# Kernel tuning notes

Hardware: AMD Instinct MI355X
Metric: run time of the kernel (lower is better)

The kernel has to match this reference:

```python
import math
import jax, jax.numpy as jnp
import numpy as np

B, L, D, H, NL, V = 4, 1024, 1024, 16, 8, 32000
HD = D // H
EPS = 1e-5


def _sinusoidal_pe(length, dim):
    pos = jnp.arange(length, dtype=jnp.float32)[:, None]
    div = jnp.exp(jnp.arange(0, dim, 2, dtype=jnp.float32) * (-math.log(10000.0) / dim))
    pe = jnp.zeros((length, dim), dtype=jnp.float32)
    pe = pe.at[:, 0::2].set(jnp.sin(pos * div))
    pe = pe.at[:, 1::2].set(jnp.cos(pos * div))
    return pe


def _layer_norm(x, scale, bias):
    mu = jnp.mean(x, axis=-1, keepdims=True)
    var = jnp.mean(jnp.square(x - mu), axis=-1, keepdims=True)
    return (x - mu) * jax.lax.rsqrt(var + EPS) * scale + bias


def setup_inputs() -> dict:
    key = jax.random.key(0)
    ks = jax.random.split(key, 10)
    std = 0.02
    p = {
        "idx": jax.random.randint(ks[0], (B, L), 0, V),
        "emb": jax.random.normal(ks[1], (V, D), jnp.float32) * std,
        # per-layer stacked params (leading dim NL)
        "ln1_s": jnp.ones((NL, D), jnp.float32),
        "ln1_b": jnp.zeros((NL, D), jnp.float32),
        "wq": jax.random.normal(ks[2], (NL, D, D), jnp.float32) * std,
        "wk": jax.random.normal(ks[3], (NL, D, D), jnp.float32) * std,
        "wv": jax.random.normal(ks[4], (NL, D, D), jnp.float32) * std,
        "wo": jax.random.normal(ks[5], (NL, D, D), jnp.float32) * std,
        "ln2_s": jnp.ones((NL, D), jnp.float32),
        "ln2_b": jnp.zeros((NL, D), jnp.float32),
        "w1": jax.random.normal(ks[6], (NL, D, 4 * D), jnp.float32) * std,
        "b1": jnp.zeros((NL, 4 * D), jnp.float32),
        "w2": jax.random.normal(ks[7], (NL, 4 * D, D), jnp.float32) * std,
        "b2": jnp.zeros((NL, D), jnp.float32),
        "lnf_s": jnp.ones((D,), jnp.float32),
        "lnf_b": jnp.zeros((D,), jnp.float32),
        "head": jax.random.normal(ks[8], (D, V), jnp.float32) * std,
    }
    return p


def _forward(idx, emb, ln1_s, ln1_b, wq, wk, wv, wo, ln2_s, ln2_b, w1, b1, w2, b2, lnf_s, lnf_b, head):
    x = emb[idx] + _sinusoidal_pe(L, D)[None]  # [B,L,D]
    causal = jnp.tril(jnp.ones((L, L), dtype=bool))  # [L,L]
    neg_inf = jnp.float32(-jnp.inf)

    def block(x, p):
        (l1s, l1b, Wq, Wk, Wv, Wo, l2s, l2b, W1, B1, W2, B2) = p
        h = _layer_norm(x, l1s, l1b)
        q = (h @ Wq).reshape(B, L, H, HD)
        k = (h @ Wk).reshape(B, L, H, HD)
        v = (h @ Wv).reshape(B, L, H, HD)
        att = jnp.einsum("bihd,bjhd->bhij", q, k) / math.sqrt(HD)
        att = jnp.where(causal, att, neg_inf)
        att = jax.nn.softmax(att, axis=-1)
        y = jnp.einsum("bhij,bjhd->bihd", att, v).reshape(B, L, D)
        x = x + y @ Wo
        h = _layer_norm(x, l2s, l2b)
        x = x + jax.nn.gelu(h @ W1 + B1, approximate=False) @ W2 + B2
        return x, None

    params = (ln1_s, ln1_b, wq, wk, wv, wo, ln2_s, ln2_b, w1, b1, w2, b2)
    x, _ = jax.lax.scan(block, x, params)
    x = _layer_norm(x, lnf_s, lnf_b)
    return x @ head  # [B,L,V]


def reference(idx, emb, ln1_s, ln1_b, wq, wk, wv, wo, ln2_s, ln2_b, w1, b1, w2, b2, lnf_s, lnf_b, head):
    return _forward(idx, emb, ln1_s, ln1_b, wq, wk, wv, wo, ln2_s, ln2_b, w1, b1, w2, b2, lnf_s, lnf_b, head)
```

## Files before the change

kernel.cpp:

```cpp
#include <hip/hip_runtime.h>
#include <hip/hip_bf16.h>
#include <math.h>

typedef __bf16 bf16_t;
typedef __attribute__((ext_vector_type(8))) __bf16 bf16x8;
typedef __attribute__((ext_vector_type(4))) float f32x4;

#define B_  4
#define L_  1024
#define D_  1024
#define H_  16
#define HD_ 64
#define NL_ 8
#define V_  32000
#define FF_ 4096

__global__ __launch_bounds__(256) void embed_kernel(const int* __restrict__ idx,
                                                    const float* __restrict__ emb,
                                                    float* __restrict__ x) {
  int token = blockIdx.x;
  int l = token & (L_ - 1);
  int id = idx[token];
  const float* erow = emb + (size_t)id * D_;
  float* xrow = x + (size_t)token * D_;
  int d0 = threadIdx.x * 4;
#pragma unroll
  for (int j = 0; j < 4; ++j) {
    int d = d0 + j;
    int i = d >> 1;
    float freq = expf((float)(2 * i) * (-9.210340371976184f / (float)D_));
    float ang = (float)l * freq;
    float pe = (d & 1) ? cosf(ang) : sinf(ang);
    xrow[d] = erow[d] + pe;
  }
}

__global__ __launch_bounds__(256) void ln_kernel(const float* __restrict__ x,
                                                 const float* __restrict__ gamma,
                                                 const float* __restrict__ beta,
                                                 bf16_t* __restrict__ out) {
  int row = blockIdx.x;
  int t = threadIdx.x;
  float4 v = ((const float4*)(x + (size_t)row * D_))[t];
  float va[4] = {v.x, v.y, v.z, v.w};
  float s = va[0] + va[1] + va[2] + va[3];
  float ss = va[0]*va[0] + va[1]*va[1] + va[2]*va[2] + va[3]*va[3];
#pragma unroll
  for (int m = 1; m < 64; m <<= 1) {
    s  += __shfl_xor(s, m);
    ss += __shfl_xor(ss, m);
  }
  __shared__ float red[8];
  int wid = t >> 6, lane = t & 63;
  if (lane == 0) { red[wid] = s; red[4 + wid] = ss; }
  __syncthreads();
  s  = red[0] + red[1] + red[2] + red[3];
  ss = red[4] + red[5] + red[6] + red[7];
  float mu  = s * (1.0f / D_);
  float var = fmaxf(ss * (1.0f / D_) - mu * mu, 0.0f);
  float rstd = rsqrtf(var + 1e-5f);
  int d0 = t * 4;
  bf16_t* orow = out + (size_t)row * D_ + d0;
#pragma unroll
  for (int j = 0; j < 4; ++j) {
    int d = d0 + j;
    orow[j] = (bf16_t)((va[j] - mu) * rstd * gamma[d] + beta[d]);
  }
}

__global__ void transpose_k(const float* __restrict__ in, size_t base,
                            bf16_t* __restrict__ out, int K, int N, int ldin) {
  __shared__ bf16_t tile[32][33];
  int n0 = blockIdx.x * 32, k0 = blockIdx.y * 32;
#pragma unroll
  for (int r = 0; r < 4; ++r) {
    int kk = threadIdx.y + r * 8;
    tile[kk][threadIdx.x] = (bf16_t)in[base + (size_t)(k0 + kk) * ldin + n0 + threadIdx.x];
  }
  __syncthreads();
#pragma unroll
  for (int r = 0; r < 4; ++r) {
    int nn = threadIdx.y + r * 8;
    out[(size_t)(n0 + nn) * K + k0 + threadIdx.x] = tile[threadIdx.x][nn];
  }
}

__global__ void transpose_layer(const float* __restrict__ wq, const float* __restrict__ wk,
                                const float* __restrict__ wv, const float* __restrict__ wo,
                                const float* __restrict__ w1, const float* __restrict__ w2,
                                size_t wofD, size_t wofF,
                                bf16_t* __restrict__ qkvT, bf16_t* __restrict__ woT,
                                bf16_t* __restrict__ w1T, bf16_t* __restrict__ w2T) {
  int t = blockIdx.x;
  const float* in; bf16_t* out; int K, N, ldin, x, y;
  if (t < 3072) {
    int z = t >> 10, tt = t & 1023;
    in = (z == 0 ? wq : z == 1 ? wk : wv) + wofD;
    out = qkvT + (size_t)z * D_ * D_;
    K = D_; N = D_; ldin = D_; x = tt & 31; y = tt >> 5;
  } else if (t < 4096) {
    int tt = t - 3072;
    in = wo + wofD; out = woT;
    K = D_; N = D_; ldin = D_; x = tt & 31; y = tt >> 5;
  } else if (t < 8192) {
    int tt = t - 4096;
    in = w1 + wofF; out = w1T;
    K = D_; N = FF_; ldin = FF_; x = tt & 127; y = tt >> 7;
  } else {
    int tt = t - 8192;
    in = w2 + wofF; out = w2T;
    K = FF_; N = D_; ldin = D_; x = tt & 31; y = tt >> 5;
  }
  __shared__ bf16_t tile[32][33];
  int n0 = x * 32, k0 = y * 32;
#pragma unroll
  for (int r = 0; r < 4; ++r) {
    int kk = threadIdx.y + r * 8;
    tile[kk][threadIdx.x] = (bf16_t)in[(size_t)(k0 + kk) * ldin + n0 + threadIdx.x];
  }
  __syncthreads();
#pragma unroll
  for (int r = 0; r < 4; ++r) {
    int nn = threadIdx.y + r * 8;
    out[(size_t)(n0 + nn) * K + k0 + threadIdx.x] = tile[threadIdx.x][nn];
  }
}

__device__ __forceinline__ void gload_lds16(const bf16_t* g, bf16_t* lds) {
  __builtin_amdgcn_global_load_lds(
      (const __attribute__((address_space(1))) void*)g,
      (__attribute__((address_space(3))) void*)(void*)lds,
      16, 0, 0);
}

__device__ __forceinline__ void remap_block(int& bn, int& bm) {
  const int gx = gridDim.x, gy = gridDim.y;
  int lin = blockIdx.y * gx + blockIdx.x;
  int nwg = gx * gy;
  int q8 = nwg >> 3, r8 = nwg & 7;
  int xcd = lin & 7, pos = lin >> 3;
  int wg = (xcd < r8 ? xcd * (q8 + 1) : r8 * (q8 + 1) + (xcd - r8) * q8) + pos;
  if ((gy & 7) == 0) {
    int per = gx << 3;
    int grp = wg / per, win = wg % per;
    bm = (grp << 3) + (win & 7);
    bn = win >> 3;
  } else { bn = wg % gx; bm = wg / gx; }
}

template <int EPI>
__global__ __launch_bounds__(256) void gemm_bt_kernel(
    const bf16_t* __restrict__ A, const bf16_t* __restrict__ Bt,
    bf16_t* __restrict__ outb, float* __restrict__ outf,
    const float* __restrict__ bias, int M, int Nst, int K, int col0) {
  int bn, bm; remap_block(bn, bm);
  const int kz = blockIdx.z, KS = gridDim.z;
  const int Kc = K / KS;
  const int kbeg = kz * Kc, kend = kbeg + Kc;
  const int tid = threadIdx.x, wid = tid >> 6, lane = tid & 63;
  const int wm = wid >> 1, wn = wid & 1;
  const int l15 = lane & 15, l4 = lane >> 4;

  __shared__ __align__(16) bf16_t As[128 * 32];
  __shared__ __align__(16) bf16_t Bs[128 * 32];

  f32x4 acc[4][4] = {};

  const bf16_t* Ablk = A  + (size_t)(bm * 128) * K;
  const bf16_t* Bblk = Bt + (size_t)(bn * 128) * K;
  const int srow = lane >> 2;
  const int skof = (lane & 3) * 8;

  for (int k0 = kbeg; k0 < kend; k0 += 32) {
#pragma unroll
    for (int c = 0; c < 2; ++c) {
      int chunk = wid * 2 + c;
      int row = chunk * 16 + srow;
      gload_lds16(Ablk + (size_t)row * K + k0 + skof, As + chunk * 512);
      gload_lds16(Bblk + (size_t)row * K + k0 + skof, Bs + chunk * 512);
    }
    __syncthreads();

    bf16x8 af[4], bfv[4];
#pragma unroll
    for (int i = 0; i < 4; ++i)
      af[i] = *(const bf16x8*)(As + (wm * 64 + i * 16 + l15) * 32 + l4 * 8);
#pragma unroll
    for (int j = 0; j < 4; ++j)
      bfv[j] = *(const bf16x8*)(Bs + (wn * 64 + j * 16 + l15) * 32 + l4 * 8);
#pragma unroll
    for (int i = 0; i < 4; ++i)
#pragma unroll
      for (int j = 0; j < 4; ++j)
        acc[i][j] = __builtin_amdgcn_mfma_f32_16x16x32_bf16(af[i], bfv[j], acc[i][j], 0, 0, 0);
    __syncthreads();
  }

  const int row_base = bm * 128 + wm * 64;
  const int col_base = col0 + bn * 128 + wn * 64 + l15;
#pragma unroll
  for (int i = 0; i < 4; ++i) {
#pragma unroll
    for (int j = 0; j < 4; ++j) {
      int col = col_base + j * 16;
#pragma unroll
      for (int r = 0; r < 4; ++r) {
        int row = row_base + i * 16 + l4 * 4 + r;
        float val = acc[i][j][r];
        if (EPI == 3 && kz == 0) val += bias[col];
        atomicAdd(&outf[(size_t)row * Nst + col], val);
      }
    }
  }
}

template <int EPI>
__global__ __launch_bounds__(512, 2) void gemm256_kernel(
    const bf16_t* __restrict__ A, const bf16_t* __restrict__ Bt,
    bf16_t* __restrict__ outb, float* __restrict__ outf,
    const float* __restrict__ bias, int M, int Nst, int K, int col0) {
  int bn, bm; remap_block(bn, bm);
  const int tid = threadIdx.x, wid = tid >> 6, lane = tid & 63;
  const int wm = wid >> 2, wn = wid & 3;
  const int l15 = lane & 15, l4 = lane >> 4;

  __shared__ __align__(16) bf16_t smem[65536];

  f32x4 acc[8][4] = {};

  const bf16_t* Ab = A  + (size_t)(bm * 256) * K;
  const bf16_t* Bb = Bt + (size_t)(bn * 256) * K;
  const int NT = K >> 6;

  const int srow = tid >> 3;
  const int sx8  = tid & 7;
  const int xrd  = l15 & 7;

  auto stage_rows = [&](int t, int mat, int R) {
    const bf16_t* g = mat ? Bb : Ab;
    bf16_t* l = smem + (t & 1) * 32768 + mat * 16384 + R * 64;
    int row = R + srow;
    int gs  = sx8 ^ (row & 7);
    gload_lds16(g + (size_t)row * K + t * 64 + gs * 8, l + wid * 512);
  };
  auto stA_SP0 = [&](int t) { stage_rows(t, 0, 0);   stage_rows(t, 0, 128); };
  auto stA_SP1 = [&](int t) { stage_rows(t, 0, 64);  stage_rows(t, 0, 192); };
  auto stB_H0  = [&](int t) { stage_rows(t, 1, 0);   stage_rows(t, 1, 64);  };
  auto stB_H1  = [&](int t) { stage_rows(t, 1, 128); stage_rows(t, 1, 192); };

  stA_SP0(0); stB_H0(0); stA_SP1(0); stB_H1(0);
  stA_SP0(1); stB_H0(1); stA_SP1(1);
  asm volatile("s_waitcnt vmcnt(6)" ::: "memory");
  __builtin_amdgcn_s_barrier();

  bf16x8 af[4][2], bfr[4][2];

  auto rdB = [&](const bf16_t* sB, int nh) {
#pragma unroll
    for (int n = 0; n < 2; ++n)
#pragma unroll
      for (int ks = 0; ks < 2; ++ks)
        bfr[nh * 2 + n][ks] = *(const bf16x8*)(sB + (wn * 64 + (nh * 2 + n) * 16 + l15) * 64
                                                  + ((ks * 4 + l4) ^ xrd) * 8);
  };
  auto rdA = [&](const bf16_t* sA, int mh) {
#pragma unroll
    for (int m = 0; m < 4; ++m)
#pragma unroll
      for (int ks = 0; ks < 2; ++ks)
        af[m][ks] = *(const bf16x8*)(sA + (wm * 128 + mh * 64 + m * 16 + l15) * 64
                                        + ((ks * 4 + l4) ^ xrd) * 8);
  };
  auto mma = [&](int mh, int nh) {
    asm volatile("s_waitcnt lgkmcnt(0)" ::: "memory");
    __builtin_amdgcn_sched_barrier(0);
    __builtin_amdgcn_s_setprio(1);
#pragma unroll
    for (int m = 0; m < 4; ++m)
#pragma unroll
      for (int n = 0; n < 2; ++n)
#pragma unroll
        for (int ks = 0; ks < 2; ++ks)
          acc[mh * 4 + m][nh * 2 + n] = __builtin_amdgcn_mfma_f32_16x16x32_bf16(
              af[m][ks], bfr[nh * 2 + n][ks], acc[mh * 4 + m][nh * 2 + n], 0, 0, 0);
    __builtin_amdgcn_s_setprio(0);
  };

  const int NI = NT >> 1;
  for (int it = 0; it < NI; ++it) {
    const int T0 = 2 * it, T1 = 2 * it + 1;
    const bool pre = (it + 1 < NI);
    const bf16_t* sA0 = smem;
    const bf16_t* sB0 = smem + 16384;
    const bf16_t* sA1 = smem + 32768;
    const bf16_t* sB1 = smem + 49152;

    rdB(sB0, 0); rdA(sA0, 0);
    stB_H1(T1);
    __builtin_amdgcn_s_barrier();
    mma(0, 0);
    __builtin_amdgcn_s_barrier();
    rdB(sB0, 1);
    if (pre) stA_SP0(T0 + 2);
    __builtin_amdgcn_s_barrier();
    mma(0, 1);
    __builtin_amdgcn_s_barrier();
    rdA(sA0, 1);
    if (pre) stB_H0(T0 + 2);
    __builtin_amdgcn_s_barrier();
    mma(1, 0);
    __builtin_amdgcn_s_barrier();
    if (pre) stA_SP1(T0 + 2);
    __builtin_amdgcn_s_barrier();
    mma(1, 1);
    if (pre) { asm volatile("s_waitcnt vmcnt(6)" ::: "memory"); }
    else     { asm volatile("s_waitcnt vmcnt(0)" ::: "memory"); }
    __builtin_amdgcn_s_barrier();

    rdB(sB1, 0); rdA(sA1, 0);
    if (pre) stB_H1(T0 + 2);
    __builtin_amdgcn_s_barrier();
    mma(0, 0);
    __builtin_amdgcn_s_barrier();
    rdB(sB1, 1);
    if (pre) stA_SP0(T1 + 2);
    __builtin_amdgcn_s_barrier();
    mma(0, 1);
    __builtin_amdgcn_s_barrier();
    rdA(sA1, 1);
    if (pre) stB_H0(T1 + 2);
    __builtin_amdgcn_s_barrier();
    mma(1, 0);
    __builtin_amdgcn_s_barrier();
    if (pre) stA_SP1(T1 + 2);
    __builtin_amdgcn_s_barrier();
    mma(1, 1);
    if (pre) { asm volatile("s_waitcnt vmcnt(6)" ::: "memory"); }
    __builtin_amdgcn_s_barrier();
  }

  const int row_base = bm * 256 + wm * 128;
#pragma unroll
  for (int m = 0; m < 8; ++m) {
#pragma unroll
    for (int n = 0; n < 4; ++n) {
      int colg = bn * 256 + wn * 64 + n * 16 + l15;
#pragma unroll
      for (int r = 0; r < 4; ++r) {
        int row = row_base + m * 16 + l4 * 4 + r;
        float val = acc[m][n][r];
        if (EPI == 4) {
          outf[(size_t)row * Nst + col0 + colg] = val;
        } else if (EPI == 2) {
          int col = col0 + colg;
          float v2 = val + bias[col];
          v2 = 0.5f * v2 * (1.0f + erff(v2 * 0.7071067811865475f));
          outb[(size_t)row * Nst + col] = (bf16_t)v2;
        } else {
          int buf = colg >> 10;
          int lc  = colg & 1023;
          (outb + (size_t)buf * 4194304)[(size_t)row * 1024 + lc] = (bf16_t)val;
        }
      }
    }
  }
}

__global__ __launch_bounds__(256) void attn_kernel(
    const bf16_t* __restrict__ q, const bf16_t* __restrict__ k,
    const bf16_t* __restrict__ v, bf16_t* __restrict__ y) {
  int bid = blockIdx.x;
  int qt = bid & 15;
  int h  = (bid >> 4) & (H_ - 1);
  int b  = bid >> 8;
  int tid = threadIdx.x, wid = tid >> 6, lane = tid & 63;
  int l15 = lane & 15, l4 = lane >> 4;

  __shared__ __align__(16) bf16_t Ks[64 * 72];
  __shared__ __align__(16) bf16_t Vs[64 * 72];
  __shared__ __align__(16) bf16_t Ps[4][16 * 72];

  const int qrow0 = qt * 64 + wid * 16;
  const size_t bh = ((size_t)b * L_ * H_ + h) * HD_;

  bf16x8 qf[2];
#pragma unroll
  for (int c = 0; c < 2; ++c)
    qf[c] = *(const bf16x8*)(q + bh + (size_t)(qrow0 + l15) * (H_ * HD_) + c * 32 + l4 * 8);

  float m_r[4] = {-INFINITY, -INFINITY, -INFINITY, -INFINITY};
  float l_r[4] = {0.f, 0.f, 0.f, 0.f};
  f32x4 oacc[4] = {};

  for (int kt = 0; kt <= qt; ++kt) {
    __syncthreads();
    int kbase = kt * 64;
#pragma unroll
    for (int s = 0; s < 2; ++s) {
      int seg = s * 256 + tid;
      int j = seg >> 3;
      int dof = (seg & 7) * 8;
      const size_t src = bh + (size_t)(kbase + j) * (H_ * HD_) + dof;
      *(bf16x8*)(Ks + j * 72 + dof) = *(const bf16x8*)(k + src);
      bf16x8 vv = *(const bf16x8*)(v + src);
      int colb = (j + dof) & 63;
#pragma unroll
      for (int jj = 0; jj < 8; ++jj) Vs[(dof + jj) * 72 + colb] = vv[jj];
    }
    __syncthreads();

    f32x4 sacc[4] = {};
#pragma unroll
    for (int c = 0; c < 2; ++c) {
#pragma unroll
      for (int t = 0; t < 4; ++t) {
        bf16x8 kf = *(const bf16x8*)(Ks + (t * 16 + l15) * 72 + c * 32 + l4 * 8);
        sacc[t] = __builtin_amdgcn_mfma_f32_16x16x32_bf16(qf[c], kf, sacc[t], 0, 0, 0);
      }
    }

    float tmax[4] = {-INFINITY, -INFINITY, -INFINITY, -INFINITY};
#pragma unroll
    for (int t = 0; t < 4; ++t) {
#pragma unroll
      for (int r = 0; r < 4; ++r) {
        float sv = sacc[t][r] * 0.125f;
        int kj = kbase + t * 16 + l15;
        int qi = qrow0 + l4 * 4 + r;
        if (kj > qi) sv = -INFINITY;
        sacc[t][r] = sv;
        tmax[r] = fmaxf(tmax[r], sv);
      }
    }
#pragma unroll
    for (int r = 0; r < 4; ++r) {
#pragma unroll
      for (int md = 1; md < 16; md <<= 1)
        tmax[r] = fmaxf(tmax[r], __shfl_xor(tmax[r], md));
    }
    float alpha[4], tsum[4];
#pragma unroll
    for (int r = 0; r < 4; ++r) {
      float mn = fmaxf(m_r[r], tmax[r]);
      alpha[r] = expf(m_r[r] - mn);
      m_r[r] = mn;
      tsum[r] = 0.f;
    }
#pragma unroll
    for (int t = 0; t < 4; ++t) {
#pragma unroll
      for (int r = 0; r < 4; ++r) {
        float p = expf(sacc[t][r] - m_r[r]);
        tsum[r] += p;
        Ps[wid][(l4 * 4 + r) * 72 + t * 16 + l15] = (bf16_t)p;
      }
    }
#pragma unroll
    for (int r = 0; r < 4; ++r) {
#pragma unroll
      for (int md = 1; md < 16; md <<= 1)
        tsum[r] += __shfl_xor(tsum[r], md);
      l_r[r] = l_r[r] * alpha[r] + tsum[r];
    }
#pragma unroll
    for (int t = 0; t < 4; ++t)
#pragma unroll
      for (int r = 0; r < 4; ++r)
        oacc[t][r] *= alpha[r];

#pragma unroll
    for (int c = 0; c < 2; ++c) {
      bf16x8 pf = *(const bf16x8*)(&Ps[wid][l15 * 72 + c * 32 + l4 * 8]);
#pragma unroll
      for (int t = 0; t < 4; ++t) {
        int d = t * 16 + l15;
        int jb = c * 32 + l4 * 8;
        bf16x8 vf = *(const bf16x8*)(Vs + d * 72 + ((jb + (d & 56)) & 63));
        oacc[t] = __builtin_amdgcn_mfma_f32_16x16x32_bf16(pf, vf, oacc[t], 0, 0, 0);
      }
    }
  }

#pragma unroll
  for (int t = 0; t < 4; ++t) {
#pragma unroll
    for (int r = 0; r < 4; ++r) {
      int row = qrow0 + l4 * 4 + r;
      int d = t * 16 + l15;
      y[bh + (size_t)row * (H_ * HD_) + d] = (bf16_t)(oacc[t][r] / l_r[r]);
    }
  }
}

extern "C" void kernel_launch(void* const* d_in, const int* in_sizes, int n_in,
                              void* d_out, int out_size, void* d_ws, size_t ws_size,
                              hipStream_t stream) {
  (void)in_sizes; (void)n_in; (void)out_size;
  const int*   idx   = (const int*)d_in[0];
  const float* emb   = (const float*)d_in[1];
  const float* ln1_s = (const float*)d_in[2];
  const float* ln1_b = (const float*)d_in[3];
  const float* wq    = (const float*)d_in[4];
  const float* wk    = (const float*)d_in[5];
  const float* wv    = (const float*)d_in[6];
  const float* wo    = (const float*)d_in[7];
  const float* ln2_s = (const float*)d_in[8];
  const float* ln2_b = (const float*)d_in[9];
  const float* w1    = (const float*)d_in[10];
  const float* b1    = (const float*)d_in[11];
  const float* w2    = (const float*)d_in[12];
  const float* b2    = (const float*)d_in[13];
  const float* lnf_s = (const float*)d_in[14];
  const float* lnf_b = (const float*)d_in[15];
  const float* headw = (const float*)d_in[16];
  float* out = (float*)d_out;

  char* ws = (char*)d_ws;
  const size_t XO  = 0;
  const size_t HBO = XO  + 16777216;
  const size_t QBO = HBO + 8388608;
  const size_t KBO = QBO + 8388608;
  const size_t VBO = KBO + 8388608;
  const size_t YBO = VBO + 8388608;
  const size_t GBO = QBO;
  const size_t WTO = YBO + 8388608;
  const size_t QKVT = WTO;
  const size_t WOT  = QKVT + 6291456;
  const size_t W1T  = WOT + 2097152;
  const size_t W2T  = W1T + 8388608;
  const size_t HDT  = WTO;

  float*  X   = (float*)(ws + XO);
  bf16_t* Hb  = (bf16_t*)(ws + HBO);
  bf16_t* Qb  = (bf16_t*)(ws + QBO);
  bf16_t* Kb  = (bf16_t*)(ws + KBO);
  bf16_t* Vb  = (bf16_t*)(ws + VBO);
  bf16_t* Yb  = (bf16_t*)(ws + YBO);
  bf16_t* Gb  = (bf16_t*)(ws + GBO);
  bf16_t* qkvT = (bf16_t*)(ws + QKVT);
  bf16_t* woT  = (bf16_t*)(ws + WOT);
  bf16_t* w1T  = (bf16_t*)(ws + W1T);
  bf16_t* w2T  = (bf16_t*)(ws + W2T);
  bf16_t* WT   = (bf16_t*)(ws + HDT);

  const int M = B_ * L_;
  const dim3 tb(32, 8);

  embed_kernel<<<M, 256, 0, stream>>>(idx, emb, X);

  for (int l = 0; l < NL_; ++l) {
    const size_t wofD = (size_t)l * D_ * D_;
    const size_t wofF = (size_t)l * D_ * FF_;

    ln_kernel<<<M, 256, 0, stream>>>(X, ln1_s + (size_t)l * D_, ln1_b + (size_t)l * D_, Hb);

    transpose_layer<<<12288, tb, 0, stream>>>(wq, wk, wv, wo, w1, w2, wofD, wofF,
                                              qkvT, woT, w1T, w2T);

    gemm256_kernel<5><<<dim3(3*D_/256, M/256), 512, 0, stream>>>(Hb, qkvT, Qb, nullptr, nullptr, M, D_, D_, 0);

    attn_kernel<<<B_ * H_ * (L_/64), 256, 0, stream>>>(Qb, Kb, Vb, Yb);

    gemm_bt_kernel<1><<<dim3(D_/128, M/128, 2), 256, 0, stream>>>(Yb, woT, nullptr, X, nullptr, M, D_, D_, 0);

    ln_kernel<<<M, 256, 0, stream>>>(X, ln2_s + (size_t)l * D_, ln2_b + (size_t)l * D_, Hb);

    gemm256_kernel<2><<<dim3(FF_/256, M/256), 512, 0, stream>>>(Hb, w1T, Gb, nullptr, b1 + (size_t)l * FF_, M, FF_, D_, 0);

    gemm_bt_kernel<3><<<dim3(D_/128, M/128, 4), 256, 0, stream>>>(Gb, w2T, nullptr, X, b2 + (size_t)l * D_, M, D_, FF_, 0);
  }

  ln_kernel<<<M, 256, 0, stream>>>(X, lnf_s, lnf_b, Hb);

  size_t avail = (ws_size > HDT) ? (ws_size - HDT) : 0;
  long long maxcols = (long long)(avail / ((size_t)D_ * 2));
  int chunk = (int)((maxcols / 256) * 256);
  if (chunk > V_) chunk = V_;
  if (chunk < 256) chunk = 256;
  for (int n0 = 0; n0 < V_; n0 += chunk) {
    int nc = (V_ - n0 < chunk) ? (V_ - n0) : chunk;
    transpose_k<<<dim3(nc/32, D_/32), tb, 0, stream>>>(headw, (size_t)n0, WT, D_, nc, V_);
    gemm256_kernel<4><<<dim3(nc/256, M/256), 512, 0, stream>>>(Hb, WT, nullptr, out, nullptr, M, V_, D_, n0);
  }
}
```

Measured before the change: 2.934 ms.

## Vectorize weight transposes with 64x64 tiles and batch all layers upfront

Replaces the 32x32 scalar transpose kernels with a 64x64-tile version that loads float4 and stores bf16x4. When the workspace is large enough, all eight layers' weights are converted in a single launch before the layer loop instead of one launch per layer. The vocab-head chunk is capped at 16384 columns, giving two chunks. The goal is less memory-bound conversion overhead and fewer launches, at the cost of a much larger workspace footprint and a fallback path when it is unavailable.

```diff
diff --git a/kernel.cpp b/kernel.cpp
--- a/kernel.cpp
+++ b/kernel.cpp
@@ -4,6 +4,7 @@
 
 typedef __bf16 bf16_t;
 typedef __attribute__((ext_vector_type(8))) __bf16 bf16x8;
+typedef __attribute__((ext_vector_type(4))) __bf16 bf16x4;
 typedef __attribute__((ext_vector_type(4))) float f32x4;
 
 #define B_  4
@@ -68,62 +69,67 @@
   }
 }
 
-__global__ void transpose_k(const float* __restrict__ in, size_t base,
-                            bf16_t* __restrict__ out, int K, int N, int ldin) {
-  __shared__ bf16_t tile[32][33];
-  int n0 = blockIdx.x * 32, k0 = blockIdx.y * 32;
+__device__ __forceinline__ void tr64_body(const float* __restrict__ in, bf16_t* __restrict__ out,
+                                          int K, int ldin, int n0, int k0) {
+  __shared__ bf16_t tile[64][66];
+  int tx = threadIdx.x, ty = threadIdx.y;
 #pragma unroll
   for (int r = 0; r < 4; ++r) {
-    int kk = threadIdx.y + r * 8;
-    tile[kk][threadIdx.x] = (bf16_t)in[base + (size_t)(k0 + kk) * ldin + n0 + threadIdx.x];
+    int kk = ty + r * 16;
+    float4 v = *(const float4*)(in + (size_t)(k0 + kk) * ldin + n0 + tx * 4);
+    tile[kk][tx * 4 + 0] = (bf16_t)v.x;
+    tile[kk][tx * 4 + 1] = (bf16_t)v.y;
+    tile[kk][tx * 4 + 2] = (bf16_t)v.z;
+    tile[kk][tx * 4 + 3] = (bf16_t)v.w;
   }
   __syncthreads();
 #pragma unroll
   for (int r = 0; r < 4; ++r) {
-    int nn = threadIdx.y + r * 8;
-    out[(size_t)(n0 + nn) * K + k0 + threadIdx.x] = tile[threadIdx.x][nn];
-  }
-}
-
-__global__ void transpose_layer(const float* __restrict__ wq, const float* __restrict__ wk,
-                                const float* __restrict__ wv, const float* __restrict__ wo,
-                                const float* __restrict__ w1, const float* __restrict__ w2,
-                                size_t wofD, size_t wofF,
-                                bf16_t* __restrict__ qkvT, bf16_t* __restrict__ woT,
-                                bf16_t* __restrict__ w1T, bf16_t* __restrict__ w2T) {
-  int t = blockIdx.x;
-  const float* in; bf16_t* out; int K, N, ldin, x, y;
-  if (t < 3072) {
-    int z = t >> 10, tt = t & 1023;
+    int nn = ty + r * 16;
+    bf16x4 w;
+    w[0] = tile[tx * 4 + 0][nn];
+    w[1] = tile[tx * 4 + 1][nn];
+    w[2] = tile[tx * 4 + 2][nn];
+    w[3] = tile[tx * 4 + 3][nn];
+    *(bf16x4*)(out + (size_t)(n0 + nn) * K + k0 + tx * 4) = w;
+  }
+}
+
+__global__ void transpose64_k(const float* __restrict__ in, size_t base,
+                              bf16_t* __restrict__ out, int K, int ldin) {
+  tr64_body(in + base, out, K, ldin, blockIdx.x * 64, blockIdx.y * 64);
+}
+
+__global__ void transpose_all(const float* __restrict__ wq, const float* __restrict__ wk,
+                              const float* __restrict__ wv, const float* __restrict__ wo,
+                              const float* __restrict__ w1, const float* __restrict__ w2,
+                              int lbase, bf16_t* __restrict__ outbase, size_t lstride) {
+  int b = blockIdx.x;
+  int li = b / 3072, t = b % 3072;
+  int l = lbase + li;
+  bf16_t* wl = outbase + (size_t)li * lstride;
+  const size_t wofD = (size_t)l * D_ * D_;
+  const size_t wofF = (size_t)l * D_ * FF_;
+  const float* in; bf16_t* out; int K, ldin, x, y;
+  if (t < 768) {
+    int z = t >> 8, tt = t & 255;
     in = (z == 0 ? wq : z == 1 ? wk : wv) + wofD;
-    out = qkvT + (size_t)z * D_ * D_;
-    K = D_; N = D_; ldin = D_; x = tt & 31; y = tt >> 5;
-  } else if (t < 4096) {
-    int tt = t - 3072;
-    in = wo + wofD; out = woT;
-    K = D_; N = D_; ldin = D_; x = tt & 31; y = tt >> 5;
-  } else if (t < 8192) {
-    int tt = t - 4096;
-    in = w1 + wofF; out = w1T;
-    K = D_; N = FF_; ldin = FF_; x = tt & 127; y = tt >> 7;
+    out = wl + (size_t)z * D_ * D_;
+    K = D_; ldin = D_; x = tt & 15; y = tt >> 4;
+  } else if (t < 1024) {
+    int tt = t - 768;
+    in = wo + wofD; out = wl + 3145728;
+    K = D_; ldin = D_; x = tt & 15; y = tt >> 4;
+  } else if (t < 2048) {
+    int tt = t - 1024;
+    in = w1 + wofF; out = wl + 4194304;
+    K = D_; ldin = FF_; x = tt & 63; y = tt >> 6;
   } else {
-    int tt = t - 8192;
-    in = w2 + wofF; out = w2T;
-    K = FF_; N = D_; ldin = D_; x = tt & 31; y = tt >> 5;
-  }
-  __shared__ bf16_t tile[32][33];
-  int n0 = x * 32, k0 = y * 32;
-#pragma unroll
-  for (int r = 0; r < 4; ++r) {
-    int kk = threadIdx.y + r * 8;
-    tile[kk][threadIdx.x] = (bf16_t)in[(size_t)(k0 + kk) * ldin + n0 + threadIdx.x];
-  }
-  __syncthreads();
-#pragma unroll
-  for (int r = 0; r < 4; ++r) {
-    int nn = threadIdx.y + r * 8;
-    out[(size_t)(n0 + nn) * K + k0 + threadIdx.x] = tile[threadIdx.x][nn];
-  }
+    int tt = t - 2048;
+    in = w2 + wofF; out = wl + 8388608;
+    K = FF_; ldin = D_; x = tt & 15; y = tt >> 4;
+  }
+  tr64_body(in, out, K, ldin, x * 64, y * 64);
 }
 
 __device__ __forceinline__ void gload_lds16(const bf16_t* g, bf16_t* lds) {
@@ -524,11 +530,9 @@
   const size_t YBO = VBO + 8388608;
   const size_t GBO = QBO;
   const size_t WTO = YBO + 8388608;
-  const size_t QKVT = WTO;
-  const size_t WOT  = QKVT + 6291456;
-  const size_t W1T  = WOT + 2097152;
-  const size_t W2T  = W1T + 8388608;
-  const size_t HDT  = WTO;
+  const size_t LBYTES = 25165824;
+  const size_t LELEMS = LBYTES / 2;
+  const bool prepass = ws_size >= WTO + (size_t)NL_ * LBYTES;
 
   float*  X   = (float*)(ws + XO);
   bf16_t* Hb  = (bf16_t*)(ws + HBO);
@@ -537,25 +541,28 @@
   bf16_t* Vb  = (bf16_t*)(ws + VBO);
   bf16_t* Yb  = (bf16_t*)(ws + YBO);
   bf16_t* Gb  = (bf16_t*)(ws + GBO);
-  bf16_t* qkvT = (bf16_t*)(ws + QKVT);
-  bf16_t* woT  = (bf16_t*)(ws + WOT);
-  bf16_t* w1T  = (bf16_t*)(ws + W1T);
-  bf16_t* w2T  = (bf16_t*)(ws + W2T);
-  bf16_t* WT   = (bf16_t*)(ws + HDT);
+  bf16_t* Wbase = (bf16_t*)(ws + WTO);
+  bf16_t* WT    = (bf16_t*)(ws + WTO);
 
   const int M = B_ * L_;
-  const dim3 tb(32, 8);
+  const dim3 tb16(16, 16);
 
   embed_kernel<<<M, 256, 0, stream>>>(idx, emb, X);
 
+  if (prepass)
+    transpose_all<<<NL_ * 3072, tb16, 0, stream>>>(wq, wk, wv, wo, w1, w2, 0, Wbase, LELEMS);
+
   for (int l = 0; l < NL_; ++l) {
-    const size_t wofD = (size_t)l * D_ * D_;
-    const size_t wofF = (size_t)l * D_ * FF_;
+    bf16_t* wl = prepass ? (Wbase + (size_t)l * LELEMS) : Wbase;
+    bf16_t* qkvT = wl;
+    bf16_t* woT  = wl + 3145728;
+    bf16_t* w1T  = wl + 4194304;
+    bf16_t* w2T  = wl + 8388608;
 
     ln_kernel<<<M, 256, 0, stream>>>(X, ln1_s + (size_t)l * D_, ln1_b + (size_t)l * D_, Hb);
 
-    transpose_layer<<<12288, tb, 0, stream>>>(wq, wk, wv, wo, w1, w2, wofD, wofF,
-                                              qkvT, woT, w1T, w2T);
+    if (!prepass)
+      transpose_all<<<3072, tb16, 0, stream>>>(wq, wk, wv, wo, w1, w2, l, Wbase, 0);
 
     gemm256_kernel<5><<<dim3(3*D_/256, M/256), 512, 0, stream>>>(Hb, qkvT, Qb, nullptr, nullptr, M, D_, D_, 0);
 
@@ -572,14 +579,14 @@
 
   ln_kernel<<<M, 256, 0, stream>>>(X, lnf_s, lnf_b, Hb);
 
-  size_t avail = (ws_size > HDT) ? (ws_size - HDT) : 0;
+  size_t avail = (ws_size > WTO) ? (ws_size - WTO) : 0;
   long long maxcols = (long long)(avail / ((size_t)D_ * 2));
   int chunk = (int)((maxcols / 256) * 256);
-  if (chunk > V_) chunk = V_;
+  if (chunk > 16384) chunk = 16384;
   if (chunk < 256) chunk = 256;
   for (int n0 = 0; n0 < V_; n0 += chunk) {
     int nc = (V_ - n0 < chunk) ? (V_ - n0) : chunk;
-    transpose_k<<<dim3(nc/32, D_/32), tb, 0, stream>>>(headw, (size_t)n0, WT, D_, nc, V_);
+    transpose64_k<<<dim3(nc/64, D_/64), tb16, 0, stream>>>(headw, (size_t)n0, WT, D_, V_);
     gemm256_kernel<4><<<dim3(nc/256, M/256), 512, 0, stream>>>(Hb, WT, nullptr, out, nullptr, M, V_, D_, n0);
   }
 }
```

Result: slower. 3.028 ms (+3.2%).
